# Kernel tuning notes

Hardware: AMD Instinct MI355X
Metric: run time of the kernel (lower is better)

The kernel has to match this reference:

```python
import jax, jax.numpy as jnp
import numpy as np


def setup_inputs() -> dict:
    key = jax.random.key(0)
    k1, k2 = jax.random.split(key)
    x = jax.random.normal(k1, (4, 2048, 2048), dtype=jnp.float32)
    weight = jax.random.normal(k2, (8192, 2048), dtype=jnp.float32) * 0.02
    return {"x": x, "weight": weight, "bits": 8}


def reference(x, weight, bits):
    # ---- activation quantization (per-row int8-style) ----
    scale = jnp.clip(jnp.max(jnp.abs(x), axis=-1, keepdims=True), 1e-5)  # [..., 1]
    max_val = (1 << (bits - 1)) - 1  # 127 for 8 bits
    x_q = jnp.clip(jnp.round(x * (max_val / scale)), -max_val, max_val)

    # ---- ternary weight quantization (-1, 0, 1) ----
    w_scale = jnp.mean(jnp.abs(weight))
    w_q = jnp.where(weight > 0.5 * w_scale, 1.0, 0.0) + jnp.where(
        weight < -0.5 * w_scale, -1.0, 0.0
    )

    # ---- dequantized linear: (x_q @ (w_q * w_scale)^T) / x_scale ----
    out = jnp.einsum("bsi,oi->bso", x_q, w_q * w_scale) / scale

    # ---- squared ReLU ----
    return jnp.maximum(out, 0.0) ** 2
```

## Files before the change

### kernel.cpp

```cpp
#include <hip/hip_runtime.h>
#include <hip/hip_bf16.h>

typedef __attribute__((ext_vector_type(4))) int i32x4;
typedef __attribute__((ext_vector_type(16))) int i32x16;

#define M_DIM 8192
#define N_DIM 8192
#define K_DIM 2048
#define BK 128
#define WCOUNT (N_DIM * K_DIM)

__global__ __launch_bounds__(256) void k_abs_partial(const float* __restrict__ w,
                                                     float* __restrict__ part) {
    int tid = blockIdx.x * 256 + threadIdx.x;
    const float4* w4 = (const float4*)w;
    float s = 0.0f;
    const int total4 = WCOUNT / 4;
    for (int i = tid; i < total4; i += 2048 * 256) {
        float4 v = w4[i];
        s += fabsf(v.x) + fabsf(v.y) + fabsf(v.z) + fabsf(v.w);
    }
    #pragma unroll
    for (int off = 1; off < 64; off <<= 1) s += __shfl_xor(s, off);
    __shared__ float red[4];
    if ((threadIdx.x & 63) == 0) red[threadIdx.x >> 6] = s;
    __syncthreads();
    if (threadIdx.x == 0)
        part[blockIdx.x] = (red[0] + red[1]) + (red[2] + red[3]);
}

__global__ __launch_bounds__(256) void k_abs_final(const float* __restrict__ part,
                                                   float* __restrict__ sum) {
    int t = threadIdx.x;
    float s = 0.0f;
    #pragma unroll
    for (int i = 0; i < 8; i++) s += part[t + i * 256];
    #pragma unroll
    for (int off = 1; off < 64; off <<= 1) s += __shfl_xor(s, off);
    __shared__ float red[4];
    if ((t & 63) == 0) red[t >> 6] = s;
    __syncthreads();
    if (t == 0) sum[0] = (red[0] + red[1]) + (red[2] + red[3]);
}

__global__ __launch_bounds__(256) void k_wquant(const float* __restrict__ w,
                                                const float* __restrict__ sum,
                                                unsigned int* __restrict__ wq) {
    const float thr = 0.5f * (sum[0] * (1.0f / 16777216.0f));
    int tid = blockIdx.x * 256 + threadIdx.x;
    const float4* w4 = (const float4*)w;
    const int total4 = WCOUNT / 4;
    for (int i = tid; i < total4; i += 2048 * 256) {
        float4 v = w4[i];
        union { signed char c[4]; unsigned int u; } q;
        q.c[0] = v.x > thr ? 1 : (v.x < -thr ? -1 : 0);
        q.c[1] = v.y > thr ? 1 : (v.y < -thr ? -1 : 0);
        q.c[2] = v.z > thr ? 1 : (v.z < -thr ? -1 : 0);
        q.c[3] = v.w > thr ? 1 : (v.w < -thr ? -1 : 0);
        wq[i] = q.u;
    }
}

__global__ __launch_bounds__(256) void k_xquant(const float* __restrict__ x,
                                                signed char* __restrict__ xq,
                                                float* __restrict__ scale) {
    const int row = blockIdx.x;
    const int t = threadIdx.x;
    const float4* xr = (const float4*)(x + (size_t)row * K_DIM);
    float4 a = xr[t * 2];
    float4 b = xr[t * 2 + 1];
    float m = fmaxf(fmaxf(fmaxf(fabsf(a.x), fabsf(a.y)), fmaxf(fabsf(a.z), fabsf(a.w))),
                    fmaxf(fmaxf(fabsf(b.x), fabsf(b.y)), fmaxf(fabsf(b.z), fabsf(b.w))));
    #pragma unroll
    for (int off = 1; off < 64; off <<= 1) m = fmaxf(m, __shfl_xor(m, off));
    __shared__ float red[4];
    if ((t & 63) == 0) red[t >> 6] = m;
    __syncthreads();
    m = fmaxf(fmaxf(red[0], red[1]), fmaxf(red[2], red[3]));
    const float sc = fmaxf(m, 1e-5f);
    if (t == 0) scale[row] = sc;
    const float r = 127.0f / sc;
    float q[8] = {a.x, a.y, a.z, a.w, b.x, b.y, b.z, b.w};
    union { signed char c[8]; uint2 v; } pk;
    #pragma unroll
    for (int j = 0; j < 8; j++) {
        float v = rintf(q[j] * r);
        v = fminf(fmaxf(v, -127.0f), 127.0f);
        pk.c[j] = (signed char)v;
    }
    *(uint2*)(xq + (size_t)row * K_DIM + t * 8) = pk.v;
}

#define GLDS16(g, l)                                                                   \
    __builtin_amdgcn_global_load_lds((const __attribute__((address_space(1))) void*)(g), \
                                     (__attribute__((address_space(3))) void*)(l), 16, 0, 0)

#define AOFF(b, h) ((b) * 32768 + (h) * 16384)
#define BOFF(b, h) (65536 + (b) * 32768 + (h) * 16384)
#define SYNC do { asm volatile("s_waitcnt vmcnt(0) lgkmcnt(0)" ::: "memory");          \
        __builtin_amdgcn_sched_barrier(0); __builtin_amdgcn_s_barrier(); } while (0)

__global__ __launch_bounds__(512, 2) void k_gemm(const signed char* __restrict__ Aq,
                                                 const signed char* __restrict__ Bq,
                                                 const float* __restrict__ scale,
                                                 const float* __restrict__ sum,
                                                 float* __restrict__ out) {
    __shared__ signed char lds[131072];

    const int t = threadIdx.x;
    const int lane = t & 63;
    const int wid = t >> 6;
    const int wm = wid >> 2;
    const int wn = wid & 3;
    const int l31 = lane & 31;
    const int kg = lane >> 5;

    const int bid = blockIdx.x;
    const int xcd = bid & 7;
    const int s_ = bid >> 3;
    const int scol = s_ >> 4;
    const int w_ = s_ & 15;
    const int brow = xcd * 4 + (w_ >> 2);
    const int bcol = scol * 4 + (w_ & 3);

    const int g_ = ((t & 7) ^ ((t >> 4) & 7)) << 4;
    const size_t sa0 = (size_t)(t >> 3) * K_DIM + g_;
    const size_t sa1 = (size_t)(64 + (t >> 3)) * K_DIM + g_;
    const int dst0 = wid * 1024;
    const int dst1 = wid * 1024 + 8192;

    const signed char* Abase = Aq + (size_t)(brow * 256) * K_DIM;
    const signed char* Bbase = Bq + (size_t)(bcol * 256) * K_DIM;

#define STGH(gb, lo) do { GLDS16((gb) + sa0, lds + (lo) + dst0);                  \
                          GLDS16((gb) + sa1, lds + (lo) + dst1); } while (0)
#define STG_A(buf, kt) do { STGH(Abase + (size_t)(kt) * BK, AOFF(buf, 0));        \
        STGH(Abase + 128 * (size_t)K_DIM + (size_t)(kt) * BK, AOFF(buf, 1)); } while (0)
#define STG_B(buf, kt) do { STGH(Bbase + (size_t)(kt) * BK, BOFF(buf, 0));        \
        STGH(Bbase + 128 * (size_t)K_DIM + (size_t)(kt) * BK, BOFF(buf, 1)); } while (0)

    const int rswz = (l31 >> 1) & 7;
    const int ko0 = ((0 * 2 + kg) ^ rswz) << 4;
    const int ko1 = ((1 * 2 + kg) ^ rswz) << 4;
    const int ko2 = ((2 * 2 + kg) ^ rswz) << 4;
    const int ko3 = ((3 * 2 + kg) ^ rswz) << 4;
    const int aB0 = AOFF(0, wm) + l31 * 128;
    const int aB1 = AOFF(1, wm) + l31 * 128;
    const int bB0 = BOFF(0, wn >> 1) + ((wn & 1) * 64 + l31) * 128;
    const int bB1 = BOFF(1, wn >> 1) + ((wn & 1) * 64 + l31) * 128;

    i32x16 acc[4][2];
    #pragma unroll
    for (int m = 0; m < 4; m++)
        #pragma unroll
        for (int n = 0; n < 2; n++)
            acc[m][n] = (i32x16){0,0,0,0,0,0,0,0,0,0,0,0,0,0,0,0};
    i32x4 fA0[4], fB0[2], fA1[4], fB1[2];

#define RDS(FA, FB, ab, bb, ko) do {                                              \
        _Pragma("unroll") for (int m_ = 0; m_ < 4; m_++)                          \
            FA[m_] = *(const i32x4*)&lds[(ab) + m_ * 4096 + (ko)];                \
        _Pragma("unroll") for (int n_ = 0; n_ < 2; n_++)                          \
            FB[n_] = *(const i32x4*)&lds[(bb) + n_ * 4096 + (ko)]; } while (0)
#define MMX(FA, FB) do { __builtin_amdgcn_s_setprio(1);                           \
        _Pragma("unroll") for (int m_ = 0; m_ < 4; m_++)                          \
        _Pragma("unroll") for (int n_ = 0; n_ < 2; n_++)                          \
            acc[m_][n_] = __builtin_amdgcn_mfma_i32_32x32x32_i8(                  \
                FA[m_], FB[n_], acc[m_][n_], 0, 0, 0);                            \
        __builtin_amdgcn_s_setprio(0); } while (0)

    STG_B(0, 0);
    STG_A(0, 0);
    STG_B(1, 1);
    asm volatile("s_waitcnt vmcnt(4)" ::: "memory");
    __builtin_amdgcn_sched_barrier(0);
    __builtin_amdgcn_s_barrier();
    RDS(fA0, fB0, aB0, bB0, ko0);

    #pragma unroll 1
    for (int i = 0; i < 8; i++) {
        const int kt = 2 * i;
        STG_A(1, kt + 1);
        RDS(fA1, fB1, aB0, bB0, ko1);
        MMX(fA0, fB0);
        RDS(fA0, fB0, aB0, bB0, ko2);
        MMX(fA1, fB1);
        RDS(fA1, fB1, aB0, bB0, ko3);
        MMX(fA0, fB0);
        SYNC;
        if (i < 7) STG_B(0, kt + 2);
        RDS(fA0, fB0, aB1, bB1, ko0);
        MMX(fA1, fB1);
        if (i < 7) STG_A(0, kt + 2);
        RDS(fA1, fB1, aB1, bB1, ko1);
        MMX(fA0, fB0);
        RDS(fA0, fB0, aB1, bB1, ko2);
        MMX(fA1, fB1);
        RDS(fA1, fB1, aB1, bB1, ko3);
        MMX(fA0, fB0);
        SYNC;
        if (i < 7) {
            STG_B(1, kt + 3);
            RDS(fA0, fB0, aB0, bB0, ko0);
        }
        MMX(fA1, fB1);
    }

    const float wsc = sum[0] * (1.0f / 16777216.0f);
    const int rb = brow * 256 + wm * 128 + 4 * kg;
    const int cb = bcol * 256 + wn * 64 + l31;
    #pragma unroll
    for (int m = 0; m < 4; m++) {
        #pragma unroll
        for (int r = 0; r < 16; r++) {
            const int grow = rb + m * 32 + (r & 3) + 8 * (r >> 2);
            const float coef = wsc / scale[grow];
            #pragma unroll
            for (int n = 0; n < 2; n++) {
                float v = (float)acc[m][n][r] * coef;
                v = fmaxf(v, 0.0f);
                out[(size_t)grow * N_DIM + cb + n * 32] = v * v;
            }
        }
    }
#undef STGH
#undef STG_A
#undef STG_B
#undef RDS
#undef MMX
}

extern "C" void kernel_launch(void* const* d_in, const int* in_sizes, int n_in,
                              void* d_out, int out_size, void* d_ws, size_t ws_size,
                              hipStream_t stream) {
    const float* x = (const float*)d_in[0];
    const float* w = (const float*)d_in[1];
    float* out = (float*)d_out;

    char* ws = (char*)d_ws;
    float* sum   = (float*)ws;
    float* part  = (float*)(ws + 256);
    float* scale = (float*)(ws + 16384);
    signed char* xq = (signed char*)(ws + 65536);
    signed char* wq = (signed char*)(ws + 65536 + 16777216);

    k_abs_partial<<<2048, 256, 0, stream>>>(w, part);
    k_abs_final<<<1, 256, 0, stream>>>(part, sum);
    k_wquant<<<2048, 256, 0, stream>>>(w, sum, (unsigned int*)wq);
    k_xquant<<<M_DIM, 256, 0, stream>>>(x, xq, scale);
    k_gemm<<<dim3(1024), 512, 0, stream>>>(xq, wq, scale, sum, out);
}
```

Before: 198.6 us.

## Restructure GEMM main loop with fine-grained waitcnt and per-step barriers

Rewrites the double-buffered int8 MFMA main loop. It now issues A and B stages together, waits on partial lgkmcnt and vmcnt counters instead of full drains, and places a workgroup barrier after every MFMA group. The goal is to overlap global-to-LDS loads with compute and to avoid full-drain syncs. The trade-off is many more s_barrier calls per iteration, which could add stalls, and the correctness of the buffer reuse depends on the chosen counter values.

```diff
diff --git a/kernel.cpp b/kernel.cpp
--- a/kernel.cpp
+++ b/kernel.cpp
@@ -97,8 +97,11 @@
 
 #define AOFF(b, h) ((b) * 32768 + (h) * 16384)
 #define BOFF(b, h) (65536 + (b) * 32768 + (h) * 16384)
-#define SYNC do { asm volatile("s_waitcnt vmcnt(0) lgkmcnt(0)" ::: "memory");          \
-        __builtin_amdgcn_sched_barrier(0); __builtin_amdgcn_s_barrier(); } while (0)
+#define BAR __builtin_amdgcn_s_barrier()
+#define LGKM6 asm volatile("s_waitcnt lgkmcnt(6)" ::: "memory")
+#define LGKM0 asm volatile("s_waitcnt lgkmcnt(0)" ::: "memory")
+#define VMCNT8 asm volatile("s_waitcnt vmcnt(8)" ::: "memory")
+#define VMCNT0 asm volatile("s_waitcnt vmcnt(0)" ::: "memory")
 
 __global__ __launch_bounds__(512, 2) void k_gemm(const signed char* __restrict__ Aq,
                                                  const signed char* __restrict__ Bq,
@@ -169,41 +172,34 @@
                 FA[m_], FB[n_], acc[m_][n_], 0, 0, 0);                            \
         __builtin_amdgcn_s_setprio(0); } while (0)
 
-    STG_B(0, 0);
-    STG_A(0, 0);
-    STG_B(1, 1);
-    asm volatile("s_waitcnt vmcnt(4)" ::: "memory");
-    __builtin_amdgcn_sched_barrier(0);
-    __builtin_amdgcn_s_barrier();
-    RDS(fA0, fB0, aB0, bB0, ko0);
+    STG_A(0, 0); STG_B(0, 0);
+    STG_A(1, 1); STG_B(1, 1);
+    VMCNT8;
+    BAR;
 
     #pragma unroll 1
     for (int i = 0; i < 8; i++) {
         const int kt = 2 * i;
-        STG_A(1, kt + 1);
+        RDS(fA0, fB0, aB0, bB0, ko0);
         RDS(fA1, fB1, aB0, bB0, ko1);
-        MMX(fA0, fB0);
+        LGKM6; MMX(fA0, fB0); BAR;
         RDS(fA0, fB0, aB0, bB0, ko2);
-        MMX(fA1, fB1);
+        LGKM6; MMX(fA1, fB1); BAR;
         RDS(fA1, fB1, aB0, bB0, ko3);
-        MMX(fA0, fB0);
-        SYNC;
-        if (i < 7) STG_B(0, kt + 2);
+        LGKM6; MMX(fA0, fB0); BAR;
+        if (i < 7) { STG_A(0, kt + 2); STG_B(0, kt + 2); VMCNT8; }
+        else       { VMCNT0; }
+        LGKM0; MMX(fA1, fB1); BAR;
         RDS(fA0, fB0, aB1, bB1, ko0);
-        MMX(fA1, fB1);
-        if (i < 7) STG_A(0, kt + 2);
         RDS(fA1, fB1, aB1, bB1, ko1);
-        MMX(fA0, fB0);
+        LGKM6; MMX(fA0, fB0); BAR;
         RDS(fA0, fB0, aB1, bB1, ko2);
-        MMX(fA1, fB1);
+        LGKM6; MMX(fA1, fB1); BAR;
         RDS(fA1, fB1, aB1, bB1, ko3);
-        MMX(fA0, fB0);
-        SYNC;
-        if (i < 7) {
-            STG_B(1, kt + 3);
-            RDS(fA0, fB0, aB0, bB0, ko0);
-        }
-        MMX(fA1, fB1);
+        LGKM6; MMX(fA0, fB0); BAR;
+        if (i < 7) { STG_A(1, kt + 3); STG_B(1, kt + 3); VMCNT8; }
+        else       { VMCNT0; }
+        LGKM0; MMX(fA1, fB1); BAR;
     }
 
     const float wsc = sum[0] * (1.0f / 16777216.0f);
```

New measurement: 203.7 us. +2.6%, slower.
